# Kernel optimization log

Hardware: AMD Instinct MI355X
Metric: run time of the kernel (lower is better)

The kernel has to match this reference:

```python
import jax, jax.numpy as jnp
import numpy as np

N_HEAD = 16
MAX_SEQ_LEN = 2048
RATIO = 1
NEG_INF = -jnp.inf


def make_alibi_bias(n_head: int, max_seq_len: int, ratio: int) -> jnp.ndarray:
    # bias[t, s] = s*ratio - t, masked to -inf where > 0 (future positions)
    s = jnp.arange(max_seq_len)[None, :] * ratio            # [1, S]
    t = jnp.arange(max_seq_len * ratio)[:, None]            # [T, 1]
    bias = (s - t).astype(jnp.float32)                      # [T, S]
    bias = jnp.where(bias > 0, NEG_INF, bias)
    # per-head slopes: cumprod of 2^(-8/n_head) -> m_i = 2^(-8*(i+1)/n_head)
    m = jnp.cumprod(jnp.full((n_head,), 2.0 ** (-8.0 / n_head), dtype=jnp.float32))
    return bias[None, :, :] * m[:, None, None]              # [H, T, S]


def setup_inputs() -> dict:
    key = jax.random.key(0)
    kq, kk, kv = jax.random.split(key, 3)
    B, T, D = 2, 2048, 1024
    return {
        "q": jax.random.normal(kq, (B, T, D), dtype=jnp.float32),
        "k": jax.random.normal(kk, (B, T, D), dtype=jnp.float32),
        "v": jax.random.normal(kv, (B, T, D), dtype=jnp.float32),
    }


def reference(q, k, v):
    B, T, D = q.shape
    S = k.shape[1]
    H = N_HEAD
    dh = D // H
    # split heads: [B, T, D] -> [B, H, T, dh]
    qh = q.reshape(B, T, H, dh).transpose(0, 2, 1, 3)
    kh = k.reshape(B, S, H, dh).transpose(0, 2, 1, 3)
    vh = v.reshape(B, S, H, dh).transpose(0, 2, 1, 3)

    scores = jnp.einsum("bhtd,bhsd->bhts", qh, kh) / jnp.sqrt(jnp.float32(dh))
    bias = make_alibi_bias(H, MAX_SEQ_LEN, RATIO)[:, -T:, -S:]  # [H, T, S]
    attn = jax.nn.softmax(scores + bias[None], axis=-1)
    out = jnp.einsum("bhts,bhsd->bhtd", attn, vh)
    # gather heads: [B, H, T, dh] -> [B, T, D]
    return out.transpose(0, 2, 1, 3).reshape(B, T, D)
```

## Files before the change

### kernel.cpp

```cpp
#include <hip/hip_runtime.h>

#define N_HEAD 16
#define DHEAD 64
#define TSEQ 2048
#define DMODEL 1024
#define BATCH 2

typedef _Float16 f16x8 __attribute__((ext_vector_type(8)));
typedef _Float16 f16x4 __attribute__((ext_vector_type(4)));
typedef _Float16 f16x2 __attribute__((ext_vector_type(2)));
typedef __fp16 fp16x2 __attribute__((ext_vector_type(2)));
typedef float f32x4 __attribute__((ext_vector_type(4)));

union F8 { f16x8 v; uint4 u; f16x2 h[4]; };
union F4 { f16x4 v; uint2 u; f16x2 h[2]; };

#if __has_builtin(__builtin_amdgcn_exp2f)
#define EXP2F(x) __builtin_amdgcn_exp2f(x)
#else
#define EXP2F(x) exp2f(x)
#endif

__device__ __forceinline__ void gload_lds16(const void* g, void* l) {
    __builtin_amdgcn_global_load_lds(
        (const __attribute__((address_space(1))) void*)g,
        (__attribute__((address_space(3))) void*)l, 16, 0, 0);
}

__device__ __forceinline__ f16x2 pk(float a, float b) {
    union { fp16x2 i; f16x2 o; } c;
    c.i = __builtin_amdgcn_cvt_pkrtz(a, b);
    return c.o;
}

__device__ __forceinline__ F8 pack8_f32(const float* p) {
    const float4 a = *(const float4*)p;
    const float4 b = *(const float4*)(p + 4);
    F8 r;
    r.h[0] = pk(a.x, a.y); r.h[1] = pk(a.z, a.w);
    r.h[2] = pk(b.x, b.y); r.h[3] = pk(b.z, b.w);
    return r;
}

__global__ __launch_bounds__(256) void prep(const float* __restrict__ K,
                                            const float* __restrict__ V,
                                            _Float16* __restrict__ Kh,
                                            _Float16* __restrict__ Vh)
{
    __shared__ float tl[64][65];
    const int bh = blockIdx.y, b = bh >> 4, h = bh & 15;
    const int s0 = blockIdx.x * 64;
    const int t = threadIdx.x;
    const int r16 = t >> 4, c4 = (t & 15) * 4;
    #pragma unroll
    for (int pass = 0; pass < 4; ++pass) {
        const int row = pass * 16 + r16;
        const size_t goff = ((size_t)(b * TSEQ + s0 + row)) * DMODEL + h * DHEAD + c4;
        const float4 fk = *(const float4*)(K + goff);
        F4 ok;
        ok.h[0] = pk(fk.x, fk.y);
        ok.h[1] = pk(fk.z, fk.w);
        *(uint2*)(Kh + (((size_t)bh * TSEQ + s0 + row) << 6) + c4) = ok.u;
        const float4 fv = *(const float4*)(V + goff);
        tl[row][c4 + 0] = fv.x; tl[row][c4 + 1] = fv.y;
        tl[row][c4 + 2] = fv.z; tl[row][c4 + 3] = fv.w;
    }
    __syncthreads();
    const int d = t >> 2, sc = (t & 3) * 16;
    F8 p0, p1;
    #pragma unroll
    for (int j = 0; j < 4; ++j) p0.h[j] = pk(tl[sc + 2 * j][d], tl[sc + 2 * j + 1][d]);
    #pragma unroll
    for (int j = 0; j < 4; ++j) p1.h[j] = pk(tl[sc + 8 + 2 * j][d], tl[sc + 9 + 2 * j][d]);
    _Float16* vo = Vh + ((size_t)bh * DHEAD + d) * TSEQ + s0 + sc;
    *(uint4*)vo = p0.u;
    *(uint4*)(vo + 8) = p1.u;
}

__global__ __launch_bounds__(128, 2) void alibi_attn(
    const float* __restrict__ Q, const _Float16* __restrict__ Kh,
    const _Float16* __restrict__ Vh, float* __restrict__ O)
{
    __shared__ __align__(16) char kbuf[2][8192];
    __shared__ __align__(16) char vbuf[2][8192];

    const int wv   = threadIdx.x >> 6;
    const int lane = threadIdx.x & 63;
    const int quad = lane >> 4;
    const int l16  = lane & 15;

    const int bh = blockIdx.x;
    const int b  = bh >> 4, h = bh & 15;
    const int sy = blockIdx.y;
    const int sx = (sy < 16) ? (31 - sy) : (sy - 16);

    const float LOG2E   = 1.44269504088896f;
    const float slope   = exp2f(-0.5f * (float)(h + 1));
    const float bslope2 = slope * LOG2E;
    const float sscale2 = 0.125f * LOG2E;
    const float step64  = 64.0f * bslope2;

    const float* qp  = Q + (size_t)b * TSEQ * DMODEL + (size_t)h * DHEAD;
    const char*  kpb = (const char*)(Kh + (size_t)bh * TSEQ * DHEAD);
    const char*  vpb = (const char*)(Vh + (size_t)bh * DHEAD * TSEQ);

    const int base_w = sx * 64 + wv * 32;

    const int st_r = lane >> 3;
    const int k_src = st_r * 128  + (((lane & 7) ^ st_r) * 16);
    const int v_src = st_r * 4096 + (((lane & 7) ^ st_r) * 16);

    auto stage = [&](int t) {
        const char* kg = kpb + (size_t)t * 8192;
        const char* vg = vpb + (size_t)t * 128;
        char* kd = kbuf[t & 1];
        char* vd = vbuf[t & 1];
        #pragma unroll
        for (int c = 0; c < 4; ++c) {
            const int gr = wv * 32 + c * 8;
            gload_lds16(kg + gr * 128 + k_src, kd + gr * 128);
            gload_lds16(vg + gr * 4096 + v_src, vd + gr * 128);
        }
    };

    stage(0);

    F8 aq[2][2];
    #pragma unroll
    for (int qs = 0; qs < 2; ++qs) {
        const float* qr = qp + (size_t)(base_w + qs * 16 + l16) * DMODEL + quad * 8;
        aq[qs][0] = pack8_f32(qr);
        aq[qs][1] = pack8_f32(qr + 32);
    }

    const int koff0 = l16 * 128 + ((quad ^ (l16 & 7)) * 16);
    const int koff1 = l16 * 128 + (((quad + 4) ^ (l16 & 7)) * 16);
    const int vbase = l16 * 128 + (quad & 1) * 8;
    int vx[4];
    #pragma unroll
    for (int sj = 0; sj < 4; ++sj)
        vx[sj] = ((sj * 2 + (quad >> 1)) ^ (l16 & 7)) * 16;

    const f32x4 zero4 = {0.f, 0.f, 0.f, 0.f};
    f32x4 o[2][4];
    float lp[2] = {0.f, 0.f};
    float dbq[2][4];
    float rb1 = bslope2, rb2 = 2.f * bslope2, rb3 = 3.f * bslope2;
    #pragma unroll
    for (int qs = 0; qs < 2; ++qs) {
        #pragma unroll
        for (int nt = 0; nt < 4; ++nt) o[qs][nt] = zero4;
        #pragma unroll
        for (int sj = 0; sj < 4; ++sj)
            dbq[qs][sj] = (float)(sj * 16 + quad * 4 - base_w - qs * 16 - l16) * bslope2;
    }

    __syncthreads();

    for (int t = 0; t <= sx; ++t) {
        if (t < sx) stage(t + 1);
        const char* kb = kbuf[t & 1];
        const char* vb = vbuf[t & 1];

        F8 kA[4][2];
        #pragma unroll
        for (int sj = 0; sj < 4; ++sj) {
            kA[sj][0].u = *(const uint4*)(kb + sj * 2048 + koff0);
            kA[sj][1].u = *(const uint4*)(kb + sj * 2048 + koff1);
        }

        f32x4 sT[2][4];
        #pragma unroll
        for (int qs = 0; qs < 2; ++qs)
            #pragma unroll
            for (int sj = 0; sj < 4; ++sj) {
                f32x4 acc = zero4;
                acc = __builtin_amdgcn_mfma_f32_16x16x32_f16(kA[sj][0].v, aq[qs][0].v, acc, 0, 0, 0);
                acc = __builtin_amdgcn_mfma_f32_16x16x32_f16(kA[sj][1].v, aq[qs][1].v, acc, 0, 0, 0);
                sT[qs][sj] = acc;
            }

        F4 vf[4][4];
        #pragma unroll
        for (int nt = 0; nt < 4; ++nt)
            #pragma unroll
            for (int sj = 0; sj < 4; ++sj)
                vf[nt][sj].u = *(const uint2*)(vb + nt * 2048 + vbase + vx[sj]);

        const bool masked = (t == sx);
        F4 pP[2][4];
        #pragma unroll
        for (int qs = 0; qs < 2; ++qs)
            #pragma unroll
            for (int sj = 0; sj < 4; ++sj) {
                const float db = dbq[qs][sj];
                float p0 = EXP2F(fmaf(sT[qs][sj][0], sscale2, db));
                float p1 = EXP2F(fmaf(sT[qs][sj][1], sscale2, db + rb1));
                float p2 = EXP2F(fmaf(sT[qs][sj][2], sscale2, db + rb2));
                float p3 = EXP2F(fmaf(sT[qs][sj][3], sscale2, db + rb3));
                if (masked) {
                    const int di = t * 64 + sj * 16 + quad * 4 - base_w - qs * 16 - l16;
                    if (di + 0 > 0) p0 = 0.f;
                    if (di + 1 > 0) p1 = 0.f;
                    if (di + 2 > 0) p2 = 0.f;
                    if (di + 3 > 0) p3 = 0.f;
                }
                lp[qs] += (p0 + p1) + (p2 + p3);
                pP[qs][sj].h[0] = pk(p0, p1);
                pP[qs][sj].h[1] = pk(p2, p3);
                dbq[qs][sj] = db + step64;
            }

        #pragma unroll
        for (int qs = 0; qs < 2; ++qs)
            #pragma unroll
            for (int nt = 0; nt < 4; ++nt)
                #pragma unroll
                for (int sj = 0; sj < 4; ++sj)
                    o[qs][nt] = __builtin_amdgcn_mfma_f32_16x16x16f16(
                        pP[qs][sj].v, vf[nt][sj].v, o[qs][nt], 0, 0, 0);

        __syncthreads();
    }

    #pragma unroll
    for (int qs = 0; qs < 2; ++qs) {
        float ls = lp[qs];
        ls += __shfl_xor(ls, 16);
        ls += __shfl_xor(ls, 32);
        float lr[4];
        #pragma unroll
        for (int r = 0; r < 4; ++r)
            lr[r] = __shfl(ls, quad * 4 + r);
        #pragma unroll
        for (int nt = 0; nt < 4; ++nt)
            #pragma unroll
            for (int r = 0; r < 4; ++r) {
                const int trow = base_w + qs * 16 + quad * 4 + r;
                O[((size_t)b * TSEQ + trow) * DMODEL + h * DHEAD + nt * 16 + l16] =
                    o[qs][nt][r] / lr[r];
            }
    }
}

extern "C" void kernel_launch(void* const* d_in, const int* in_sizes, int n_in,
                              void* d_out, int out_size, void* d_ws, size_t ws_size,
                              hipStream_t stream) {
    const float* q = (const float*)d_in[0];
    const float* k = (const float*)d_in[1];
    const float* v = (const float*)d_in[2];
    float* out = (float*)d_out;

    _Float16* Kh = (_Float16*)d_ws;
    _Float16* Vh = Kh + (size_t)BATCH * N_HEAD * TSEQ * DHEAD;

    prep<<<dim3(TSEQ / 64, BATCH * N_HEAD), 256, 0, stream>>>(k, v, Kh, Vh);
    alibi_attn<<<dim3(BATCH * N_HEAD, 32), 128, 0, stream>>>(q, Kh, Vh, out);
}
```

Measured before the change: 135.1 us.

## Pair causal tiles per block with four waves of sixteen query rows

Result: faster. 127.3 us (-5.8%).

```diff
diff --git a/kernel.cpp b/kernel.cpp
--- a/kernel.cpp
+++ b/kernel.cpp
@@ -47,7 +47,7 @@
                                             _Float16* __restrict__ Kh,
                                             _Float16* __restrict__ Vh)
 {
-    __shared__ float tl[64][65];
+    __shared__ float tl[64][67];
     const int bh = blockIdx.y, b = bh >> 4, h = bh & 15;
     const int s0 = blockIdx.x * 64;
     const int t = threadIdx.x;
@@ -77,7 +77,7 @@
     *(uint4*)(vo + 8) = p1.u;
 }
 
-__global__ __launch_bounds__(128, 2) void alibi_attn(
+__global__ __launch_bounds__(256, 2) void alibi_attn(
     const float* __restrict__ Q, const _Float16* __restrict__ Kh,
     const _Float16* __restrict__ Vh, float* __restrict__ O)
 {
@@ -91,47 +91,22 @@
 
     const int bh = blockIdx.x;
     const int b  = bh >> 4, h = bh & 15;
-    const int sy = blockIdx.y;
-    const int sx = (sy < 16) ? (31 - sy) : (sy - 16);
+    const int px = blockIdx.y;
 
     const float LOG2E   = 1.44269504088896f;
     const float slope   = exp2f(-0.5f * (float)(h + 1));
     const float bslope2 = slope * LOG2E;
     const float sscale2 = 0.125f * LOG2E;
     const float step64  = 64.0f * bslope2;
+    const float rb1 = bslope2, rb2 = 2.f * bslope2, rb3 = 3.f * bslope2;
 
     const float* qp  = Q + (size_t)b * TSEQ * DMODEL + (size_t)h * DHEAD;
     const char*  kpb = (const char*)(Kh + (size_t)bh * TSEQ * DHEAD);
     const char*  vpb = (const char*)(Vh + (size_t)bh * DHEAD * TSEQ);
 
-    const int base_w = sx * 64 + wv * 32;
-
-    const int st_r = lane >> 3;
+    const int st_r  = lane >> 3;
     const int k_src = st_r * 128  + (((lane & 7) ^ st_r) * 16);
     const int v_src = st_r * 4096 + (((lane & 7) ^ st_r) * 16);
-
-    auto stage = [&](int t) {
-        const char* kg = kpb + (size_t)t * 8192;
-        const char* vg = vpb + (size_t)t * 128;
-        char* kd = kbuf[t & 1];
-        char* vd = vbuf[t & 1];
-        #pragma unroll
-        for (int c = 0; c < 4; ++c) {
-            const int gr = wv * 32 + c * 8;
-            gload_lds16(kg + gr * 128 + k_src, kd + gr * 128);
-            gload_lds16(vg + gr * 4096 + v_src, vd + gr * 128);
-        }
-    };
-
-    stage(0);
-
-    F8 aq[2][2];
-    #pragma unroll
-    for (int qs = 0; qs < 2; ++qs) {
-        const float* qr = qp + (size_t)(base_w + qs * 16 + l16) * DMODEL + quad * 8;
-        aq[qs][0] = pack8_f32(qr);
-        aq[qs][1] = pack8_f32(qr + 32);
-    }
 
     const int koff0 = l16 * 128 + ((quad ^ (l16 & 7)) * 16);
     const int koff1 = l16 * 128 + (((quad + 4) ^ (l16 & 7)) * 16);
@@ -142,90 +117,102 @@
         vx[sj] = ((sj * 2 + (quad >> 1)) ^ (l16 & 7)) * 16;
 
     const f32x4 zero4 = {0.f, 0.f, 0.f, 0.f};
-    f32x4 o[2][4];
-    float lp[2] = {0.f, 0.f};
-    float dbq[2][4];
-    float rb1 = bslope2, rb2 = 2.f * bslope2, rb3 = 3.f * bslope2;
-    #pragma unroll
-    for (int qs = 0; qs < 2; ++qs) {
-        #pragma unroll
-        for (int nt = 0; nt < 4; ++nt) o[qs][nt] = zero4;
+
+    for (int hp = 0; hp < 2; ++hp) {
+        const int sx     = hp ? (31 - px) : px;
+        const int base_w = sx * 64 + wv * 16;
+
+        auto stage = [&](int t) {
+            const char* kg = kpb + (size_t)t * 8192;
+            const char* vg = vpb + (size_t)t * 128;
+            char* kd = kbuf[t & 1];
+            char* vd = vbuf[t & 1];
+            #pragma unroll
+            for (int c = 0; c < 2; ++c) {
+                const int gr = wv * 16 + c * 8;
+                gload_lds16(kg + gr * 128 + k_src, kd + gr * 128);
+                gload_lds16(vg + gr * 4096 + v_src, vd + gr * 128);
+            }
+        };
+
+        stage(0);
+
+        const float* qr = qp + (size_t)(base_w + l16) * DMODEL + quad * 8;
+        const F8 aq0 = pack8_f32(qr);
+        const F8 aq1 = pack8_f32(qr + 32);
+
+        f32x4 o[4];
+        float lp = 0.f;
+        float dbq[4];
+        #pragma unroll
+        for (int nt = 0; nt < 4; ++nt) o[nt] = zero4;
         #pragma unroll
         for (int sj = 0; sj < 4; ++sj)
-            dbq[qs][sj] = (float)(sj * 16 + quad * 4 - base_w - qs * 16 - l16) * bslope2;
-    }
-
-    __syncthreads();
-
-    for (int t = 0; t <= sx; ++t) {
-        if (t < sx) stage(t + 1);
-        const char* kb = kbuf[t & 1];
-        const char* vb = vbuf[t & 1];
-
-        F8 kA[4][2];
-        #pragma unroll
-        for (int sj = 0; sj < 4; ++sj) {
-            kA[sj][0].u = *(const uint4*)(kb + sj * 2048 + koff0);
-            kA[sj][1].u = *(const uint4*)(kb + sj * 2048 + koff1);
-        }
-
-        f32x4 sT[2][4];
-        #pragma unroll
-        for (int qs = 0; qs < 2; ++qs)
+            dbq[sj] = (float)(sj * 16 + quad * 4 - base_w - l16) * bslope2;
+
+        __syncthreads();
+
+        for (int t = 0; t <= sx; ++t) {
+            if (t < sx) stage(t + 1);
+            const char* kb = kbuf[t & 1];
+            const char* vb = vbuf[t & 1];
+
+            F8 kA[4][2];
+            #pragma unroll
+            for (int sj = 0; sj < 4; ++sj) {
+                kA[sj][0].u = *(const uint4*)(kb + sj * 2048 + koff0);
+                kA[sj][1].u = *(const uint4*)(kb + sj * 2048 + koff1);
+            }
+
+            f32x4 sT[4];
             #pragma unroll
             for (int sj = 0; sj < 4; ++sj) {
                 f32x4 acc = zero4;
-                acc = __builtin_amdgcn_mfma_f32_16x16x32_f16(kA[sj][0].v, aq[qs][0].v, acc, 0, 0, 0);
-                acc = __builtin_amdgcn_mfma_f32_16x16x32_f16(kA[sj][1].v, aq[qs][1].v, acc, 0, 0, 0);
-                sT[qs][sj] = acc;
-            }
-
-        F4 vf[4][4];
-        #pragma unroll
-        for (int nt = 0; nt < 4; ++nt)
-            #pragma unroll
-            for (int sj = 0; sj < 4; ++sj)
-                vf[nt][sj].u = *(const uint2*)(vb + nt * 2048 + vbase + vx[sj]);
-
-        const bool masked = (t == sx);
-        F4 pP[2][4];
-        #pragma unroll
-        for (int qs = 0; qs < 2; ++qs)
+                acc = __builtin_amdgcn_mfma_f32_16x16x32_f16(kA[sj][0].v, aq0.v, acc, 0, 0, 0);
+                acc = __builtin_amdgcn_mfma_f32_16x16x32_f16(kA[sj][1].v, aq1.v, acc, 0, 0, 0);
+                sT[sj] = acc;
+            }
+
+            F4 vf[4][4];
+            #pragma unroll
+            for (int nt = 0; nt < 4; ++nt)
+                #pragma unroll
+                for (int sj = 0; sj < 4; ++sj)
+                    vf[nt][sj].u = *(const uint2*)(vb + nt * 2048 + vbase + vx[sj]);
+
+            const bool masked = (t == sx);
+            F4 pP[4];
             #pragma unroll
             for (int sj = 0; sj < 4; ++sj) {
-                const float db = dbq[qs][sj];
-                float p0 = EXP2F(fmaf(sT[qs][sj][0], sscale2, db));
-                float p1 = EXP2F(fmaf(sT[qs][sj][1], sscale2, db + rb1));
-                float p2 = EXP2F(fmaf(sT[qs][sj][2], sscale2, db + rb2));
-                float p3 = EXP2F(fmaf(sT[qs][sj][3], sscale2, db + rb3));
+                const float db = dbq[sj];
+                float p0 = EXP2F(fmaf(sT[sj][0], sscale2, db));
+                float p1 = EXP2F(fmaf(sT[sj][1], sscale2, db + rb1));
+                float p2 = EXP2F(fmaf(sT[sj][2], sscale2, db + rb2));
+                float p3 = EXP2F(fmaf(sT[sj][3], sscale2, db + rb3));
                 if (masked) {
-                    const int di = t * 64 + sj * 16 + quad * 4 - base_w - qs * 16 - l16;
+                    const int di = t * 64 + sj * 16 + quad * 4 - base_w - l16;
                     if (di + 0 > 0) p0 = 0.f;
                     if (di + 1 > 0) p1 = 0.f;
                     if (di + 2 > 0) p2 = 0.f;
                     if (di + 3 > 0) p3 = 0.f;
                 }
-                lp[qs] += (p0 + p1) + (p2 + p3);
-                pP[qs][sj].h[0] = pk(p0, p1);
-                pP[qs][sj].h[1] = pk(p2, p3);
-                dbq[qs][sj] = db + step64;
-            }
-
-        #pragma unroll
-        for (int qs = 0; qs < 2; ++qs)
+                lp += (p0 + p1) + (p2 + p3);
+                pP[sj].h[0] = pk(p0, p1);
+                pP[sj].h[1] = pk(p2, p3);
+                dbq[sj] = db + step64;
+            }
+
             #pragma unroll
             for (int nt = 0; nt < 4; ++nt)
                 #pragma unroll
                 for (int sj = 0; sj < 4; ++sj)
-                    o[qs][nt] = __builtin_amdgcn_mfma_f32_16x16x16f16(
-                        pP[qs][sj].v, vf[nt][sj].v, o[qs][nt], 0, 0, 0);
-
-        __syncthreads();
-    }
-
-    #pragma unroll
-    for (int qs = 0; qs < 2; ++qs) {
-        float ls = lp[qs];
+                    o[nt] = __builtin_amdgcn_mfma_f32_16x16x16f16(
+                        pP[sj].v, vf[nt][sj].v, o[nt], 0, 0, 0);
+
+            __syncthreads();
+        }
+
+        float ls = lp;
         ls += __shfl_xor(ls, 16);
         ls += __shfl_xor(ls, 32);
         float lr[4];
@@ -236,9 +223,9 @@
         for (int nt = 0; nt < 4; ++nt)
             #pragma unroll
             for (int r = 0; r < 4; ++r) {
-                const int trow = base_w + qs * 16 + quad * 4 + r;
+                const int trow = base_w + quad * 4 + r;
                 O[((size_t)b * TSEQ + trow) * DMODEL + h * DHEAD + nt * 16 + l16] =
-                    o[qs][nt][r] / lr[r];
+                    o[nt][r] / lr[r];
             }
     }
 }
@@ -255,5 +242,5 @@
     _Float16* Vh = Kh + (size_t)BATCH * N_HEAD * TSEQ * DHEAD;
 
     prep<<<dim3(TSEQ / 64, BATCH * N_HEAD), 256, 0, stream>>>(k, v, Kh, Vh);
-    alibi_attn<<<dim3(BATCH * N_HEAD, 32), 128, 0, stream>>>(q, Kh, Vh, out);
-}
+    alibi_attn<<<dim3(BATCH * N_HEAD, 16), 256, 0, stream>>>(q, Kh, Vh, out);
+}
```
